# Optimization experiments

Measured on AMD Instinct MI355X. Metric: run time of the kernel, lower is better.

The kernel has to match this reference:

```python
import jax, jax.numpy as jnp
import numpy as np

N_HEADS = 8
D_EMBED = 1024
D_CROSS = 768
D_HEAD = D_EMBED // N_HEADS


def setup_inputs() -> dict:
    key = jax.random.key(0)
    ks = jax.random.split(key, 10)
    B, SQ, SKV = 8, 4096, 77
    scale_e = 1.0 / np.sqrt(D_EMBED)
    scale_c = 1.0 / np.sqrt(D_CROSS)
    return {
        "x": jax.random.normal(ks[0], (B, SQ, D_EMBED), dtype=jnp.float32),
        "y": jax.random.normal(ks[1], (B, SKV, D_CROSS), dtype=jnp.float32),
        # weights stored as [in, out] so projection is x @ W + b
        "Wq": jax.random.normal(ks[2], (D_EMBED, D_EMBED), dtype=jnp.float32) * scale_e,
        "bq": jnp.zeros((D_EMBED,), dtype=jnp.float32),
        "Wk": jax.random.normal(ks[3], (D_CROSS, D_EMBED), dtype=jnp.float32) * scale_c,
        "bk": jnp.zeros((D_EMBED,), dtype=jnp.float32),
        "Wv": jax.random.normal(ks[4], (D_CROSS, D_EMBED), dtype=jnp.float32) * scale_c,
        "bv": jnp.zeros((D_EMBED,), dtype=jnp.float32),
        "Wo": jax.random.normal(ks[5], (D_EMBED, D_EMBED), dtype=jnp.float32) * scale_e,
        "bo": jnp.zeros((D_EMBED,), dtype=jnp.float32),
    }


def reference(x, y, Wq, bq, Wk, bk, Wv, bv, Wo, bo):
    B, SQ, _ = x.shape
    # projections
    q = x @ Wq + bq                      # [B, SQ, D_EMBED]
    k = y @ Wk + bk                      # [B, SKV, D_EMBED]
    v = y @ Wv + bv                      # [B, SKV, D_EMBED]
    # split heads -> [B, H, S, Dh]
    q = q.reshape(B, SQ, N_HEADS, D_HEAD).transpose(0, 2, 1, 3)
    k = k.reshape(B, -1, N_HEADS, D_HEAD).transpose(0, 2, 1, 3)
    v = v.reshape(B, -1, N_HEADS, D_HEAD).transpose(0, 2, 1, 3)
    # attention: q@k^T / sqrt(d_head), softmax, @v
    scale = 1.0 / jnp.sqrt(jnp.asarray(D_HEAD, dtype=q.dtype))
    weight = jnp.einsum("bhqd,bhkd->bhqk", q, k) * scale  # [B, H, SQ, SKV]
    weight = jax.nn.softmax(weight, axis=-1)
    out = jnp.einsum("bhqk,bhkd->bhqd", weight, v)        # [B, H, SQ, Dh]
    out = out.transpose(0, 2, 1, 3).reshape(B, SQ, D_EMBED)
    return out @ Wo + bo
```

## Files before the change

### kernel.cpp

```cpp
#include <hip/hip_runtime.h>

typedef _Float16 half_t;
typedef _Float16 half8 __attribute__((ext_vector_type(8)));
typedef float f32x4 __attribute__((ext_vector_type(4)));

#define D_EMBED   1024
#define D_CROSS   768
#define N_HEADS   8
#define D_HEAD    128
#define BATCH     8
#define SEQ_Q     4096
#define SEQ_KV    77
#define SKV_PAD   80
#define NKV       (N_HEADS*SKV_PAD)
#define NKV_PAD   768
#define M_Q       (BATCH*SEQ_Q)

#define WS_S     ((size_t)0)
#define WS_WQC   (WS_S    + (size_t)M_Q*NKV*2)
#define WS_WOT   (WS_WQC  + (size_t)D_EMBED*D_EMBED*2)
#define WS_WKVT  (WS_WOT  + (size_t)D_EMBED*D_EMBED*2)
#define WS_YH    (WS_WKVT + (size_t)2*D_EMBED*D_CROSS*2)
#define WS_KV    (WS_YH   + (size_t)BATCH*SKV_PAD*D_CROSS*2)
#define WS_BKV   (WS_KV   + (size_t)BATCH*SKV_PAD*2*D_EMBED*2)
#define WS_BT1   (WS_BKV  + (size_t)2*D_EMBED*4)
#define WS_BT2   (WS_BT1  + (size_t)BATCH*NKV_PAD*D_EMBED*2)
#define WS_C1    (WS_BT2  + (size_t)BATCH*D_EMBED*NKV*2)

#define ATTN_SCALE 0.08838834764831845f

__device__ __forceinline__ void gload_lds16(const void* g, void* lds) {
  __builtin_amdgcn_global_load_lds(
      (const __attribute__((address_space(1))) unsigned int*)g,
      (__attribute__((address_space(3))) unsigned int*)lds, 16, 0, 0);
}
__device__ __forceinline__ void BAR() {
  __builtin_amdgcn_s_barrier();
  __builtin_amdgcn_sched_barrier(0);
}

__global__ void cast_f32_f16(const float* __restrict__ src, half_t* __restrict__ dst) {
  int i = blockIdx.x * 256 + threadIdx.x;
  f32x4 a = *(const f32x4*)(src + (size_t)i*8);
  f32x4 b = *(const f32x4*)(src + (size_t)i*8 + 4);
  half8 h;
#pragma unroll
  for (int j = 0; j < 4; ++j) { h[j] = (half_t)a[j]; h[j+4] = (half_t)b[j]; }
  *(half8*)(dst + (size_t)i*8) = h;
}

__global__ void transpose_f32f16(const float* __restrict__ src, half_t* __restrict__ dst,
                                 int K, int N) {
  __shared__ float tile[32][33];
  int n0 = blockIdx.x * 32, k0 = blockIdx.y * 32;
  int tx = threadIdx.x, ty = threadIdx.y;
#pragma unroll
  for (int j = 0; j < 4; ++j)
    tile[ty + j*8][tx] = src[(size_t)(k0 + ty + j*8)*N + n0 + tx];
  __syncthreads();
#pragma unroll
  for (int j = 0; j < 4; ++j)
    dst[(size_t)(n0 + ty + j*8)*K + k0 + tx] = (half_t)tile[tx][ty + j*8];
}

__global__ void convert_pad_y(const float* __restrict__ y, half_t* __restrict__ yh) {
  int idx = blockIdx.x * 256 + threadIdx.x;
  int r = idx / D_CROSS, col = idx - r*D_CROSS;
  int b = r / SKV_PAD, s = r - b*SKV_PAD;
  yh[idx] = (s < SEQ_KV) ? (half_t)y[(size_t)(b*SEQ_KV + s)*D_CROSS + col] : (half_t)0.f;
}

__global__ void concat_bias(const float* __restrict__ bk, const float* __restrict__ bv,
                            float* __restrict__ bkv) {
  int i = blockIdx.x * 256 + threadIdx.x;
  bkv[i] = (i < D_EMBED) ? bk[i] : bv[i - D_EMBED];
}

__global__ __launch_bounds__(256, 3)
void gemm_kv(const half_t* __restrict__ A, const half_t* __restrict__ Bt,
             const float* __restrict__ bias, half_t* __restrict__ C,
             int M, int N, int K) {
  __shared__ half_t As[3][128*32];
  __shared__ half_t Bs[2][128*32];
  const int tid = threadIdx.x;
  const int l = tid & 63, w = tid >> 6;
  const int l4 = l & 15, lh = l >> 4;
  const int bn0 = blockIdx.x * 128, bm0 = blockIdx.y * 128;
  const int wr = w >> 1, wc = w & 1;
  const int rslot = lh << 4;
  f32x4 acc[4][4] = {};
  const int nk = K >> 5;
  const int srow = w*16 + (l >> 2);
  const int scol = (l & 3)*8;

  auto stageB = [&](int kt, int bb) {
    const half_t* g = Bt + (size_t)(bn0 + srow)*K + scol + kt*32;
    gload_lds16(g,                 (char*)Bs[bb] + w*1024);
    gload_lds16(g + (size_t)64*K,  (char*)Bs[bb] + 4096 + w*1024);
  };
  auto stageA = [&](int kt, int bb) {
    const half_t* g = A + (size_t)(bm0 + srow)*K + scol + kt*32;
    gload_lds16(g,                 (char*)As[bb] + w*1024);
    gload_lds16(g + (size_t)64*K,  (char*)As[bb] + 4096 + w*1024);
  };
  auto compute = [&](int ab, int bb) {
    half8 af[4], bf[4];
#pragma unroll
    for (int m = 0; m < 4; ++m)
      af[m] = *(const half8*)((const char*)As[ab] + (size_t)(wr*64 + m*16 + l4)*64 + rslot);
#pragma unroll
    for (int n = 0; n < 4; ++n)
      bf[n] = *(const half8*)((const char*)Bs[bb] + (size_t)(wc*64 + n*16 + l4)*64 + rslot);
#pragma unroll
    for (int m = 0; m < 4; ++m)
#pragma unroll
      for (int n = 0; n < 4; ++n)
        acc[m][n] = __builtin_amdgcn_mfma_f32_16x16x32_f16(af[m], bf[n], acc[m][n], 0, 0, 0);
  };

  stageA(0, 0); stageA(1, 1); stageB(0, 0);
  asm volatile("s_waitcnt vmcnt(0)" ::: "memory");
  BAR();
  int aCur = 0, aP2 = 2;
  for (int t = 0; t < nk; ++t) {
    if (t + 1 < nk) stageB(t + 1, (t + 1) & 1);
    if (t + 2 < nk) stageA(t + 2, aP2);
    compute(aCur, t & 1);
    if (t + 1 < nk) {
      if (t + 2 < nk) { asm volatile("s_waitcnt vmcnt(2)" ::: "memory"); }
      else            { asm volatile("s_waitcnt vmcnt(0)" ::: "memory"); }
      BAR();
    }
    aCur = (aCur == 2) ? 0 : aCur + 1;
    aP2  = (aP2  == 2) ? 0 : aP2  + 1;
  }

  const int cb = bn0 + wc*64, rb = bm0 + wr*64;
#pragma unroll
  for (int n = 0; n < 4; ++n) {
    const int col = cb + n*16 + l4;
    const float bvv = bias[col];
#pragma unroll
    for (int m = 0; m < 4; ++m)
#pragma unroll
      for (int j = 0; j < 4; ++j)
        C[(size_t)(rb + m*16 + lh*4 + j)*N + col] = (half_t)(acc[m][n][j] + bvv);
  }
}

__global__ __launch_bounds__(256, 2)
void w1_build(const half_t* __restrict__ kvb, const half_t* __restrict__ Wqc,
              half_t* __restrict__ Bt1) {
  __shared__ half_t K_lds[80*136];
  const int blk = blockIdx.x;
  const int b = blk >> 3, h = blk & 7;
  const int tid = threadIdx.x;
  const int l = tid & 63, w = tid >> 6;
  const int l4 = l & 15, lh = l >> 4;
  for (int i = tid; i < 80*16; i += 256) {
    int s = i >> 4, d = (i & 15) << 3;
    *(half8*)(K_lds + s*136 + d) =
        *(const half8*)(kvb + (size_t)(b*SKV_PAD + s)*2048 + h*128 + d);
  }
  __syncthreads();
  for (int c = 0; c < 4; ++c) {
    f32x4 acc[5][4] = {};
#pragma unroll
    for (int kt = 0; kt < 4; ++kt) {
      half8 af[5], bf[4];
#pragma unroll
      for (int m = 0; m < 5; ++m)
        af[m] = *(const half8*)(K_lds + (size_t)(m*16 + l4)*136 + kt*32 + lh*8);
#pragma unroll
      for (int n = 0; n < 4; ++n)
        bf[n] = *(const half8*)(Wqc + (size_t)(w*256 + c*64 + n*16 + l4)*1024 + h*128 + kt*32 + lh*8);
#pragma unroll
      for (int m = 0; m < 5; ++m)
#pragma unroll
        for (int n = 0; n < 4; ++n)
          acc[m][n] = __builtin_amdgcn_mfma_f32_16x16x32_f16(af[m], bf[n], acc[m][n], 0, 0, 0);
    }
#pragma unroll
    for (int n = 0; n < 4; ++n) {
      const int colk = w*256 + c*64 + n*16 + l4;
#pragma unroll
      for (int m = 0; m < 5; ++m)
#pragma unroll
        for (int j = 0; j < 4; ++j) {
          const int r = h*SKV_PAD + m*16 + lh*4 + j;
          size_t byte = ((size_t)(b*NKV_PAD + r))*2048 + (size_t)(colk >> 6)*128
                        + ((size_t)(((colk >> 3) & 7) ^ (r & 7)) << 4) + ((colk & 7) << 1);
          *(half_t*)((char*)Bt1 + byte) = (half_t)(acc[m][n][j]*ATTN_SCALE);
        }
    }
  }
}

__global__ __launch_bounds__(256, 2)
void w2_build(const half_t* __restrict__ kvb, const half_t* __restrict__ Wot,
              half_t* __restrict__ Bt2) {
  __shared__ half_t V_lds[80*136];
  const int blk = blockIdx.x;
  const int b = blk >> 3, h = blk & 7;
  const int tid = threadIdx.x;
  const int l = tid & 63, w = tid >> 6;
  const int l4 = l & 15, lh = l >> 4;
  for (int i = tid; i < 80*16; i += 256) {
    int s = i >> 4, d = (i & 15) << 3;
    *(half8*)(V_lds + s*136 + d) =
        *(const half8*)(kvb + (size_t)(b*SKV_PAD + s)*2048 + 1024 + h*128 + d);
  }
  __syncthreads();
  for (int c = 0; c < 4; ++c) {
    f32x4 acc[4][5] = {};
#pragma unroll
    for (int kt = 0; kt < 4; ++kt) {
      half8 af[4], bf[5];
#pragma unroll
      for (int m = 0; m < 4; ++m)
        af[m] = *(const half8*)(Wot + (size_t)(w*256 + c*64 + m*16 + l4)*1024 + h*128 + kt*32 + lh*8);
#pragma unroll
      for (int n = 0; n < 5; ++n)
        bf[n] = *(const half8*)(V_lds + (size_t)(n*16 + l4)*136 + kt*32 + lh*8);
#pragma unroll
      for (int m = 0; m < 4; ++m)
#pragma unroll
        for (int n = 0; n < 5; ++n)
          acc[m][n] = __builtin_amdgcn_mfma_f32_16x16x32_f16(af[m], bf[n], acc[m][n], 0, 0, 0);
    }
#pragma unroll
    for (int m = 0; m < 4; ++m) {
#pragma unroll
      for (int j = 0; j < 4; ++j) {
        const int nrow = w*256 + c*64 + m*16 + lh*4 + j;
        const size_t rowbase = ((size_t)(b*1024 + nrow))*1280;
#pragma unroll
        for (int n = 0; n < 5; ++n) {
          const int cc = h*80 + n*16 + l4;
          size_t byte = rowbase + (size_t)(cc >> 6)*128
                        + ((size_t)(((cc >> 3) & 7) ^ (nrow & 7)) << 4) + ((cc & 7) << 1);
          *(half_t*)((char*)Bt2 + byte) = (half_t)acc[m][n][j];
        }
      }
    }
  }
}

__global__ void c1_build(const half_t* __restrict__ kvb, const float* __restrict__ bq,
                         float* __restrict__ c1) {
  int idx = blockIdx.x * 256 + threadIdx.x;
  int b = idx / NKV, n = idx - b*NKV;
  int h = n / SKV_PAD, s = n - h*SKV_PAD;
  const half_t* kp = kvb + (size_t)(b*SKV_PAD + s)*2048 + h*128;
  float acc = 0.f;
#pragma unroll 8
  for (int d = 0; d < 128; ++d) acc += bq[h*128 + d] * (float)kp[d];
  c1[idx] = acc * ATTN_SCALE;
}

__global__ __launch_bounds__(512, 1)
void fused_sv(const float* __restrict__ X, const half_t* __restrict__ Bt1,
              const float* __restrict__ c1, const half_t* __restrict__ Bt2,
              const float* __restrict__ bo, float* __restrict__ out) {
  __shared__ half_t S_lds[64*640];
  __shared__ half_t x_lds[2][64*64];
  const int tid = threadIdx.x;
  const int l = tid & 63, w = tid >> 6;
  const int l4 = l & 15, lh = l >> 4;
  const int k7 = l4 & 7;

  const int lin = ((int)blockIdx.x & 7)*64 + ((int)blockIdx.x >> 3);
  const int batch = lin >> 6;
  const int row0 = batch*SEQ_Q + (lin & 63)*64;
  const char* W1 = (const char*)(Bt1 + (size_t)batch*NKV_PAD*1024);
  const char* W2 = (const char*)(Bt2 + (size_t)batch*1024*NKV);
  const float* c1b = c1 + batch*NKV;

  f32x4 sacc[4][5] = {};
  const int nfb = w*5;

  const int xrow = tid >> 3, xc8 = tid & 7;
  const float* xg = X + (size_t)(row0 + xrow)*1024 + xc8*8;
  f32x4 xa, xb;
  auto xload = [&](int kc) {
    const float* g = xg + kc*64;
    xa = *(const f32x4*)g; xb = *(const f32x4*)(g + 4);
  };
  auto xwrite = [&](int buf) {
    half8 h;
#pragma unroll
    for (int e = 0; e < 4; ++e) { h[e] = (half_t)xa[e]; h[e+4] = (half_t)xb[e]; }
    *(half8*)((char*)x_lds[buf] + xrow*128 + ((xc8 ^ (xrow & 7)) << 4)) = h;
  };

  half8 b0[5], b1[5];
  auto bload = [&](int t, half8* dst) {
    const int kc = t >> 1, kk = t & 1;
    const size_t koff = (size_t)kc*128 + (size_t)(((kk*4 + lh) ^ k7) << 4);
#pragma unroll
    for (int nf = 0; nf < 5; ++nf)
      dst[nf] = *(const half8*)(W1 + (size_t)((nfb + nf)*16 + l4)*2048 + koff);
  };
  auto smfma = [&](const half8* bf, int kc, int kk) {
    const char* xc = (const char*)x_lds[kc & 1];
    half8 af[4];
#pragma unroll
    for (int m = 0; m < 4; ++m)
      af[m] = *(const half8*)(xc + (size_t)(m*16 + l4)*128 + (((kk*4 + lh) ^ k7) << 4));
    __builtin_amdgcn_s_setprio(1);
#pragma unroll
    for (int nf = 0; nf < 5; ++nf)
#pragma unroll
      for (int m = 0; m < 4; ++m)
        sacc[m][nf] = __builtin_amdgcn_mfma_f32_16x16x32_f16(af[m], bf[nf], sacc[m][nf], 0, 0, 0);
    __builtin_amdgcn_s_setprio(0);
  };

  xload(0); xwrite(0);
  bload(0, b0);
  asm volatile("s_waitcnt lgkmcnt(0)" ::: "memory");
  BAR();

  for (int kc = 0; kc < 16; ++kc) {
    if (kc + 1 < 16) xload(kc + 1);
    bload(2*kc + 1, b1);
    smfma(b0, kc, 0);
    if (2*kc + 2 < 32) bload(2*kc + 2, b0);
    smfma(b1, kc, 1);
    if (kc + 1 < 16) {
      xwrite((kc + 1) & 1);
      asm volatile("s_waitcnt lgkmcnt(0)" ::: "memory");
      BAR();
    }
  }

#pragma unroll
  for (int nf = 0; nf < 5; ++nf) {
    const int col = (nfb + nf)*16 + l4;
#pragma unroll
    for (int m = 0; m < 4; ++m)
#pragma unroll
      for (int j = 0; j < 4; ++j) {
        const int row = m*16 + lh*4 + j;
        size_t byte = (size_t)row*1280 + (size_t)(col >> 6)*128
                      + ((size_t)(((col >> 3) & 7) ^ (row & 7)) << 4) + ((col & 7) << 1);
        *(half_t*)((char*)S_lds + byte) = (half_t)sacc[m][nf][j];
      }
  }
  asm volatile("s_waitcnt lgkmcnt(0)" ::: "memory");
  BAR();

  {
    const int row = tid >> 3, h = tid & 7;
    const int key = row & 7;
    char* base = (char*)S_lds + (size_t)row*1280;
    float fv[10][8];
    float mx = -1e30f;
#pragma unroll
    for (int i = 0; i < 10; ++i) {
      const int ls = h*10 + i;
      half8 v = *(const half8*)(base + (size_t)(ls >> 3)*128 + ((size_t)((ls & 7) ^ key) << 4));
      f32x4 ca = *(const f32x4*)(c1b + h*80 + i*8);
      f32x4 cb = *(const f32x4*)(c1b + h*80 + i*8 + 4);
#pragma unroll
      for (int j = 0; j < 8; ++j) {
        const float cc = (j < 4) ? ca[j] : cb[j - 4];
        const float sv = (float)v[j] + cc;
        const bool ok = (i*8 + j) < SEQ_KV;
        fv[i][j] = ok ? sv : -1e30f;
        if (ok) mx = fmaxf(mx, sv);
      }
    }
    float sm = 0.f;
#pragma unroll
    for (int i = 0; i < 10; ++i)
#pragma unroll
      for (int j = 0; j < 8; ++j) { float e = __expf(fv[i][j] - mx); sm += e; fv[i][j] = e; }
    const float inv = 1.f / sm;
#pragma unroll
    for (int i = 0; i < 10; ++i) {
      const int ls = h*10 + i;
      half8 t;
#pragma unroll
      for (int j = 0; j < 8; ++j) t[j] = (half_t)(fv[i][j] * inv);
      *(half8*)(base + (size_t)(ls >> 3)*128 + ((size_t)((ls & 7) ^ key) << 4)) = t;
    }
  }
  asm volatile("s_waitcnt lgkmcnt(0)" ::: "memory");
  BAR();

#pragma unroll 1
  for (int pass = 0; pass < 2; ++pass) {
    f32x4 oacc[4][4] = {};
    half8 p0[4], p1[4];
    const int ncb = w*128 + pass*64;
    auto pbload = [&](int ks, half8* dst) {
      const size_t koff = (size_t)(ks >> 1)*128 + (size_t)((((ks & 1)*4 + lh) ^ k7) << 4);
#pragma unroll
      for (int nf = 0; nf < 4; ++nf)
        dst[nf] = *(const half8*)(W2 + (size_t)(ncb + nf*16 + l4)*1280 + koff);
    };
    auto pmfma = [&](const half8* bf, int ks) {
      const size_t koff = (size_t)(ks >> 1)*128 + (size_t)((((ks & 1)*4 + lh) ^ k7) << 4);
      half8 af[4];
#pragma unroll
      for (int m = 0; m < 4; ++m)
        af[m] = *(const half8*)((const char*)S_lds + (size_t)(m*16 + l4)*1280 + koff);
      __builtin_amdgcn_s_setprio(1);
#pragma unroll
      for (int nf = 0; nf < 4; ++nf)
#pragma unroll
        for (int m = 0; m < 4; ++m)
          oacc[m][nf] = __builtin_amdgcn_mfma_f32_16x16x32_f16(af[m], bf[nf], oacc[m][nf], 0, 0, 0);
      __builtin_amdgcn_s_setprio(0);
    };

    pbload(0, p0);
    for (int ks = 0; ks < 20; ks += 2) {
      pbload(ks + 1, p1);
      pmfma(p0, ks);
      if (ks + 2 < 20) pbload(ks + 2, p0);
      pmfma(p1, ks + 1);
    }

#pragma unroll
    for (int nf = 0; nf < 4; ++nf) {
      const int col = ncb + nf*16 + l4;
      const float bvv = bo[col];
#pragma unroll
      for (int m = 0; m < 4; ++m)
#pragma unroll
        for (int j = 0; j < 4; ++j) {
          const int row = row0 + m*16 + lh*4 + j;
          out[(size_t)row*1024 + col] = oacc[m][nf][j] + bvv;
        }
    }
  }
}

extern "C" void kernel_launch(void* const* d_in, const int* in_sizes, int n_in,
                              void* d_out, int out_size, void* d_ws, size_t ws_size,
                              hipStream_t stream) {
  (void)in_sizes; (void)n_in; (void)out_size; (void)ws_size;
  const float* x  = (const float*)d_in[0];
  const float* y  = (const float*)d_in[1];
  const float* Wq = (const float*)d_in[2];
  const float* bq = (const float*)d_in[3];
  const float* Wk = (const float*)d_in[4];
  const float* bk = (const float*)d_in[5];
  const float* Wv = (const float*)d_in[6];
  const float* bv = (const float*)d_in[7];
  const float* Wo = (const float*)d_in[8];
  const float* bo = (const float*)d_in[9];

  char* ws = (char*)d_ws;
  half_t* Wqc  = (half_t*)(ws + WS_WQC);
  half_t* Wot  = (half_t*)(ws + WS_WOT);
  half_t* Wkvt = (half_t*)(ws + WS_WKVT);
  half_t* yh   = (half_t*)(ws + WS_YH);
  half_t* kvb  = (half_t*)(ws + WS_KV);
  float*  bkv  = (float*)(ws + WS_BKV);
  half_t* Bt1  = (half_t*)(ws + WS_BT1);
  half_t* Bt2  = (half_t*)(ws + WS_BT2);
  float*  c1   = (float*)(ws + WS_C1);

  dim3 tb(32, 8);
  cast_f32_f16<<<512, 256, 0, stream>>>(Wq, Wqc);
  transpose_f32f16<<<dim3(32, 32), tb, 0, stream>>>(Wo, Wot, 1024, 1024);
  transpose_f32f16<<<dim3(32, 24), tb, 0, stream>>>(Wk, Wkvt, 768, 1024);
  transpose_f32f16<<<dim3(32, 24), tb, 0, stream>>>(Wv, Wkvt + (size_t)1024*768, 768, 1024);
  convert_pad_y<<<BATCH*SKV_PAD*D_CROSS/256, 256, 0, stream>>>(y, yh);
  concat_bias<<<2*D_EMBED/256, 256, 0, stream>>>(bk, bv, bkv);

  gemm_kv<<<dim3(16, 5), 256, 0, stream>>>(yh, Wkvt, bkv, kvb, BATCH*SKV_PAD, 2048, 768);

  c1_build<<<BATCH*NKV/256, 256, 0, stream>>>(kvb, bq, c1);
  w1_build<<<BATCH*N_HEADS, 256, 0, stream>>>(kvb, Wqc, Bt1);
  w2_build<<<BATCH*N_HEADS, 256, 0, stream>>>(kvb, Wot, Bt2);

  fused_sv<<<512, 512, 0, stream>>>(x, Bt1, c1, Bt2, bo, (float*)d_out);
}
```

Before: 248.1 us.

## Double fused kernel block to 1024 threads and split work across more waves

Result: slower. 297.4 us (+19.9%).

```diff
diff --git a/kernel.cpp b/kernel.cpp
--- a/kernel.cpp
+++ b/kernel.cpp
@@ -258,7 +258,7 @@
   c1[idx] = acc * ATTN_SCALE;
 }
 
-__global__ __launch_bounds__(512, 1)
+__global__ __launch_bounds__(1024, 1)
 void fused_sv(const float* __restrict__ X, const half_t* __restrict__ Bt1,
               const float* __restrict__ c1, const half_t* __restrict__ Bt2,
               const float* __restrict__ bo, float* __restrict__ out) {
@@ -276,21 +276,28 @@
   const char* W2 = (const char*)(Bt2 + (size_t)batch*1024*NKV);
   const float* c1b = c1 + batch*NKV;
 
-  f32x4 sacc[4][5] = {};
-  const int nfb = w*5;
-
-  const int xrow = tid >> 3, xc8 = tid & 7;
-  const float* xg = X + (size_t)(row0 + xrow)*1024 + xc8*8;
-  f32x4 xa, xb;
-  auto xload = [&](int kc) {
-    const float* g = xg + kc*64;
-    xa = *(const f32x4*)g; xb = *(const f32x4*)(g + 4);
-  };
-  auto xwrite = [&](int buf) {
-    half8 h;
-#pragma unroll
-    for (int e = 0; e < 4; ++e) { h[e] = (half_t)xa[e]; h[e+4] = (half_t)xb[e]; }
-    *(half8*)((char*)x_lds[buf] + xrow*128 + ((xc8 ^ (xrow & 7)) << 4)) = h;
+  f32x4 sacc[2][5] = {};
+  const int head = w >> 1, rh = w & 1;
+  const int nfb = head*5;
+  const int mrow0 = rh*32;
+
+  const int xrow = tid >> 4, xc4 = (tid & 15)*4;
+  const float* xg = X + (size_t)(row0 + xrow)*1024 + xc4;
+  f32x4 L0v, L1v;
+  auto xload0 = [&](int kc) { L0v = *(const f32x4*)(xg + kc*64); };
+  auto xload1 = [&](int kc) { L1v = *(const f32x4*)(xg + kc*64); };
+  const int xslot = ((((xc4 >> 3) & 7) ^ (xrow & 7)) << 4) + (xc4 & 7)*2;
+  auto xwrite0 = [&](int buf) {
+    half_t h4[4];
+#pragma unroll
+    for (int e = 0; e < 4; ++e) h4[e] = (half_t)L0v[e];
+    *(uint2*)((char*)x_lds[buf] + xrow*128 + xslot) = *(const uint2*)h4;
+  };
+  auto xwrite1 = [&](int buf) {
+    half_t h4[4];
+#pragma unroll
+    for (int e = 0; e < 4; ++e) h4[e] = (half_t)L1v[e];
+    *(uint2*)((char*)x_lds[buf] + xrow*128 + xslot) = *(const uint2*)h4;
   };
 
   half8 b0[5], b1[5];
@@ -303,32 +310,37 @@
   };
   auto smfma = [&](const half8* bf, int kc, int kk) {
     const char* xc = (const char*)x_lds[kc & 1];
-    half8 af[4];
-#pragma unroll
-    for (int m = 0; m < 4; ++m)
-      af[m] = *(const half8*)(xc + (size_t)(m*16 + l4)*128 + (((kk*4 + lh) ^ k7) << 4));
+    half8 af[2];
+#pragma unroll
+    for (int m = 0; m < 2; ++m)
+      af[m] = *(const half8*)(xc + (size_t)(mrow0 + m*16 + l4)*128 + (((kk*4 + lh) ^ k7) << 4));
     __builtin_amdgcn_s_setprio(1);
 #pragma unroll
     for (int nf = 0; nf < 5; ++nf)
 #pragma unroll
-      for (int m = 0; m < 4; ++m)
+      for (int m = 0; m < 2; ++m)
         sacc[m][nf] = __builtin_amdgcn_mfma_f32_16x16x32_f16(af[m], bf[nf], sacc[m][nf], 0, 0, 0);
     __builtin_amdgcn_s_setprio(0);
   };
 
-  xload(0); xwrite(0);
+  xload0(0); xload1(1);
+  xwrite0(0);
   bload(0, b0);
   asm volatile("s_waitcnt lgkmcnt(0)" ::: "memory");
   BAR();
 
   for (int kc = 0; kc < 16; ++kc) {
-    if (kc + 1 < 16) xload(kc + 1);
+    if (kc + 1 < 16) {
+      if ((kc + 1) & 1) xwrite1((kc + 1) & 1); else xwrite0((kc + 1) & 1);
+    }
+    if (kc + 2 < 16) {
+      if (kc & 1) xload1(kc + 2); else xload0(kc + 2);
+    }
     bload(2*kc + 1, b1);
     smfma(b0, kc, 0);
     if (2*kc + 2 < 32) bload(2*kc + 2, b0);
     smfma(b1, kc, 1);
     if (kc + 1 < 16) {
-      xwrite((kc + 1) & 1);
       asm volatile("s_waitcnt lgkmcnt(0)" ::: "memory");
       BAR();
     }
@@ -338,10 +350,10 @@
   for (int nf = 0; nf < 5; ++nf) {
     const int col = (nfb + nf)*16 + l4;
 #pragma unroll
-    for (int m = 0; m < 4; ++m)
+    for (int m = 0; m < 2; ++m)
 #pragma unroll
       for (int j = 0; j < 4; ++j) {
-        const int row = m*16 + lh*4 + j;
+        const int row = mrow0 + m*16 + lh*4 + j;
         size_t byte = (size_t)row*1280 + (size_t)(col >> 6)*128
                       + ((size_t)(((col >> 3) & 7) ^ (row & 7)) << 4) + ((col & 7) << 1);
         *(half_t*)((char*)S_lds + byte) = (half_t)sacc[m][nf][j];
@@ -350,7 +362,7 @@
   asm volatile("s_waitcnt lgkmcnt(0)" ::: "memory");
   BAR();
 
-  {
+  if (tid < 512) {
     const int row = tid >> 3, h = tid & 7;
     const int key = row & 7;
     char* base = (char*)S_lds + (size_t)row*1280;
@@ -389,11 +401,10 @@
   asm volatile("s_waitcnt lgkmcnt(0)" ::: "memory");
   BAR();
 
-#pragma unroll 1
-  for (int pass = 0; pass < 2; ++pass) {
+  {
     f32x4 oacc[4][4] = {};
     half8 p0[4], p1[4];
-    const int ncb = w*128 + pass*64;
+    const int ncb = w*64;
     auto pbload = [&](int ks, half8* dst) {
       const size_t koff = (size_t)(ks >> 1)*128 + (size_t)((((ks & 1)*4 + lh) ^ k7) << 4);
 #pragma unroll
@@ -478,5 +489,5 @@
   w1_build<<<BATCH*N_HEADS, 256, 0, stream>>>(kvb, Wqc, Bt1);
   w2_build<<<BATCH*N_HEADS, 256, 0, stream>>>(kvb, Wot, Bt2);
 
-  fused_sv<<<512, 512, 0, stream>>>(x, Bt1, c1, Bt2, bo, (float*)d_out);
-}
+  fused_sv<<<512, 1024, 0, stream>>>(x, Bt1, c1, Bt2, bo, (float*)d_out);
+}
```
